# Kernel tuning notes

Hardware: AMD Instinct MI355X
Metric: run time of the kernel (lower is better)

Reference implementation:

```python
import jax, jax.numpy as jnp
import numpy as np

B = 512      # batch
T = 16       # tokens per instruction
V = 1000     # vocab
E = 4        # num_experts
K = 1        # active experts per layer
NLAYERS = 3
TOPK_LOGIC = 32


def _conv(x, w, b, stride=2):
    # x: [B,Cin,H,W], w: [Cout,Cin,3,3] (OIHW), padding=1, stride=2
    y = jax.lax.conv_general_dilated(
        x, w, window_strides=(stride, stride), padding=((1, 1), (1, 1)),
        dimension_numbers=('NCHW', 'OIHW', 'NCHW'))
    return y + b[None, :, None, None]


def _gated_conv(x, w, b, gate):
    # w: [E,Cout,Cin,3,3], b: [E,Cout], gate: [B,E] 0/1 mask
    # Faithful to original: all experts computed densely, then masked.
    outs = jax.vmap(lambda wi, bi: _conv(x, wi, bi))(w, b)  # [E,B,Cout,H',W']
    return jnp.einsum('ebchw,be->bchw', outs, gate)


def _topk_mask(logits, k):
    # 0/1 mask with ones at the top-k positions along the last axis
    _, idx = jax.lax.top_k(logits, k)
    return jnp.sum(jax.nn.one_hot(idx, logits.shape[-1], dtype=logits.dtype), axis=-2)


def setup_inputs() -> dict:
    key = jax.random.key(0)
    ks = jax.random.split(key, 16)
    def rn(k, shape, s=0.05):
        return jax.random.normal(k, shape, jnp.float32) * s
    return dict(
        img=jax.random.normal(ks[0], (B, 12, 56, 56), jnp.float32),
        text=jax.random.randint(ks[1], (B, T), 0, V),
        prev_action=jax.random.randint(ks[2], (B,), 0, 7),
        emb_table=rn(ks[3], (V, 32), 1.0),
        r_w1=rn(ks[4], (32, 64)), r_b1=jnp.zeros((64,), jnp.float32),
        r_w2=rn(ks[5], (64, NLAYERS * E)), r_b2=jnp.zeros((NLAYERS * E,), jnp.float32),
        l_w1=rn(ks[6], (32, 64)), l_b1=jnp.zeros((64,), jnp.float32),
        l_w2=rn(ks[7], (64, 256)), l_b2=jnp.zeros((256,), jnp.float32),
        c1_w=rn(ks[8], (E, 32, 12, 3, 3)), c1_b=jnp.zeros((E, 32), jnp.float32),
        c2_w=rn(ks[9], (E, 64, 32, 3, 3)), c2_b=jnp.zeros((E, 64), jnp.float32),
        c3_w=rn(ks[10], (E, 128, 64, 3, 3)), c3_b=jnp.zeros((E, 128), jnp.float32),
        act_emb=rn(ks[11], (7, 16), 1.0),
        f_w=rn(ks[12], (6272 + 32 + 16, 256)), f_b=jnp.zeros((256,), jnp.float32),
        h_w=rn(ks[13], (256, 5)), h_b=jnp.zeros((5,), jnp.float32),
    )


def reference(img, text, prev_action, emb_table, r_w1, r_b1, r_w2, r_b2,
              l_w1, l_b1, l_w2, l_b2, c1_w, c1_b, c2_w, c2_b, c3_w, c3_b,
              act_emb, f_w, f_b, h_w, h_b):
    # EmbeddingBag(mode='mean') over token dim
    lang = jnp.mean(emb_table[text], axis=1)                      # [B,32]
    # Router: MLP -> [B,3,E] logits, top-k scatter -> 0/1 mask
    rlog = (jax.nn.relu(lang @ r_w1 + r_b1) @ r_w2 + r_b2).reshape(-1, NLAYERS, E)
    masks = _topk_mask(rlog, K)                                   # [B,3,E]
    x = jax.nn.relu(_gated_conv(img, c1_w, c1_b, masks[:, 0, :])) # [B,32,28,28]
    x = jax.nn.relu(_gated_conv(x, c2_w, c2_b, masks[:, 1, :]))   # [B,64,14,14]
    x = jax.nn.relu(_gated_conv(x, c3_w, c3_b, masks[:, 2, :]))   # [B,128,7,7]
    vis = x.reshape(x.shape[0], -1)                               # [B,6272]
    act = act_emb[prev_action]                                    # [B,16]
    fused = jnp.concatenate([vis, lang, act], axis=1)             # [B,6320]
    hidden = fused @ f_w + f_b                                    # [B,256]
    logic = jax.nn.relu(lang @ l_w1 + l_b1) @ l_w2 + l_b2         # [B,256]
    lmask = _topk_mask(logic, TOPK_LOGIC)                         # [B,256]
    out = jax.nn.relu(hidden * lmask)                             # dropout is identity in eval
    logits = out @ h_w + h_b                                      # [B,5]
    return logits, rlog
```

## Files before the change

kernel.cpp:

```cpp
#include <hip/hip_runtime.h>
#include <hip/hip_bf16.h>


typedef __bf16 bf16x8 __attribute__((ext_vector_type(8)));
typedef float f32x4 __attribute__((ext_vector_type(4)));

__device__ __forceinline__ unsigned short f2bf(float f) {
  union { float f; unsigned u; } v; v.f = f;
  unsigned r = v.u + 0x7FFFu + ((v.u >> 16) & 1u);
  return (unsigned short)(r >> 16);
}

__device__ __forceinline__ int wswz(int b) { return b ^ (((b >> 7) & 3) << 4); }

__global__ __launch_bounds__(256) void prep_kernel(
    const int* __restrict__ text, const float* __restrict__ emb,
    const float* __restrict__ r_w1, const float* __restrict__ r_b1,
    const float* __restrict__ r_w2, const float* __restrict__ r_b2,
    const float* __restrict__ l_w1, const float* __restrict__ l_b1,
    const float* __restrict__ l_w2, const float* __restrict__ l_b2,
    const float* __restrict__ act_emb, const int* __restrict__ pa,
    const float* __restrict__ c1_w, const float* __restrict__ c2_w,
    const float* __restrict__ c3_w, const float* __restrict__ fw,
    float* __restrict__ rlog_out, int* __restrict__ eidx, float* __restrict__ lmask,
    unsigned short* __restrict__ tailb,
    unsigned short* __restrict__ wb1, unsigned short* __restrict__ wb2,
    unsigned short* __restrict__ wb3, unsigned short* __restrict__ fwT) {
  __shared__ __align__(16) char shm[64 * 72 * 2];
  const int blk = blockIdx.x;
  const int tid = threadIdx.x;

  if (blk < 512) {
    int b = blk;
    int t = tid;
    __shared__ float lg[32];
    __shared__ float hr[64];
    __shared__ float hl[64];
    __shared__ float rl[12];
    __shared__ float lgc[256];

    if (t < 32) {
      const int* tb = text + b * 16;
      float s = 0.f;
#pragma unroll
      for (int tok = 0; tok < 16; ++tok) s += emb[tb[tok] * 32 + t];
      lg[t] = s * 0.0625f;
    }
    __syncthreads();

    if (t < 64) {
      float s1 = r_b1[t], s2 = l_b1[t];
      for (int k = 0; k < 32; ++k) {
        float lv = lg[k];
        s1 += lv * r_w1[k * 64 + t];
        s2 += lv * l_w1[k * 64 + t];
      }
      hr[t] = fmaxf(s1, 0.f);
      hl[t] = fmaxf(s2, 0.f);
    }
    if (t < 64) {
      float v = 0.f;
      if (t < 32) v = lg[t];
      else if (t < 48) v = act_emb[pa[b] * 16 + (t - 32)];
      tailb[b * 64 + t] = f2bf(v);
    }
    __syncthreads();

    if (t < 12) {
      float s = r_b2[t];
      for (int k = 0; k < 64; ++k) s += hr[k] * r_w2[k * 12 + t];
      rl[t] = s;
      rlog_out[b * 12 + t] = s;
    }
    {
      float s = l_b2[t];
      for (int k = 0; k < 64; ++k) s += hl[k] * l_w2[k * 256 + t];
      lgc[t] = s;
    }
    __syncthreads();

    if (t < 3) {
      int best = 0;
      float bv = rl[t * 4];
      for (int e = 1; e < 4; ++e) {
        float v = rl[t * 4 + e];
        if (v > bv) { bv = v; best = e; }
      }
      eidx[b * 3 + t] = best;
    }
    {
      float v = lgc[t];
      int cnt = 0;
      for (int k = 0; k < 256; ++k) {
        float u = lgc[k];
        cnt += (u > v) || (u == v && k < t);
      }
      lmask[b * 256 + t] = (cnt < 32) ? 1.f : 0.f;
    }
  } else if (blk < 2080) {
    int idx = (blk - 512) * 256 + tid;
    if (idx < 24576) {
      int k = idx % 192, ec = idx / 192;
      float v = 0.f;
      if (k < 144) {
        int g = k >> 4, ci = k & 15;
        if (ci < 12) v = c1_w[ec * 108 + ci * 9 + g];
      }
      wb1[idx] = f2bf(v);
    } else if (idx < 106496) {
      int i2 = idx - 24576;
      int k = i2 % 320, ec = i2 / 320;
      float v = 0.f;
      if (k < 288) {
        int g = k >> 5, ci = k & 31;
        v = c2_w[ec * 288 + ci * 9 + g];
      }
      wb2[i2] = f2bf(v);
    } else {
      int i3 = idx - 106496;
      int k = i3 % 576, ec = i3 / 576;
      int g = k >> 6, ci = k & 63;
      wb3[i3] = f2bf(c3_w[ec * 576 + ci * 9 + g]);
    }
  } else {
    unsigned short(*tl)[72] = (unsigned short(*)[72])shm;
    int fb = blk - 2080;
    int kblk = fb >> 2, nblk = fb & 3;
    int n0 = nblk * 64;
    int k0 = kblk * 64;
    int rl = tid >> 2;
    int c4 = (tid & 3) * 16;
    int srow;
    bool valid;
    if (kblk < 98) {
      int p = kblk >> 1;
      int c0 = (kblk & 1) * 64;
      srow = (c0 + rl) * 49 + p;
      valid = true;
    } else {
      srow = 6272 + rl;
      valid = (rl < 48);
    }
#pragma unroll
    for (int h = 0; h < 4; ++h) {
      float4 v = valid ? *(const float4*)&fw[(size_t)srow * 256 + n0 + c4 + h * 4]
                       : (float4){0.f, 0.f, 0.f, 0.f};
      tl[rl][c4 + h * 4 + 0] = f2bf(v.x);
      tl[rl][c4 + h * 4 + 1] = f2bf(v.y);
      tl[rl][c4 + h * 4 + 2] = f2bf(v.z);
      tl[rl][c4 + h * 4 + 3] = f2bf(v.w);
    }
    __syncthreads();
    int nloc = tid >> 2;
    int kc = (tid & 3) * 16;
    unsigned short vv[16];
#pragma unroll
    for (int i = 0; i < 16; ++i) vv[i] = tl[kc + i][nloc];
    unsigned short* dst = fwT + (size_t)(n0 + nloc) * 6336 + k0 + kc;
    *(uint4*)dst = *(const uint4*)&vv[0];
    *(uint4*)(dst + 8) = *(const uint4*)&vv[8];
  }
}

__global__ __launch_bounds__(256) void bucket_kernel(const int* __restrict__ eidx,
                                                     int* __restrict__ cnt,
                                                     int* __restrict__ perm) {
  int l = blockIdx.x;
  __shared__ int el[512];
  __shared__ int cc[4];
  int t = threadIdx.x;
  el[t] = eidx[t * 3 + l];
  el[t + 256] = eidx[(t + 256) * 3 + l];
  __syncthreads();
  if (t < 4) {
    int c = 0;
    for (int b = 0; b < 512; ++b) c += (el[b] == t);
    cc[t] = c;
    cnt[l * 4 + t] = c;
  }
  __syncthreads();
#pragma unroll
  for (int rep = 0; rep < 2; ++rep) {
    int b = t + rep * 256;
    int e = el[b];
    int rank = 0;
    for (int bp = 0; bp < b; ++bp) rank += (el[bp] == e);
    int off = 0;
    for (int ee = 0; ee < e; ++ee) off += cc[ee];
    perm[l * 512 + off + rank] = b;
  }
}

__global__ __launch_bounds__(256) void conv1_fused(
    const float* __restrict__ img, const unsigned short* __restrict__ wb,
    const float* __restrict__ bias, const int* __restrict__ eidx,
    unsigned short* __restrict__ out) {
  const int s = blockIdx.x / 7;
  const int t = blockIdx.x % 7;
  const int e = eidx[s * 3];
  __shared__ __align__(16) char win[25536];
  __shared__ __align__(16) char ldsB[3 * 4096];
  const int tid = threadIdx.x;
  const int lane = tid & 63;
  const int wid = tid >> 6;
  const int wm0 = wid * 32;

  const int p0 = t * 128;
  const int ohmin = p0 / 28;
  const int ih0 = ohmin * 2 - 1;

  {
    uint4 z; z.x = z.y = z.z = z.w = 0u;
    for (int i = tid; i < 1596; i += 256) ((uint4*)win)[i] = z;
  }
  {
    const unsigned short* wbe = wb + e * (32 * 192);
#pragma unroll
    for (int c = 0; c < 3; ++c) {
      int cc = tid + 256 * c;
      int n = cc / 24, cb = cc - n * 24;
      int kt = cb >> 3, cbl = cb & 7;
      uint4 v = *(const uint4*)(wbe + n * 192 + cb * 8);
      *(uint4*)(ldsB + kt * 4096 + n * 128 + ((cbl * 16) ^ ((n & 7) << 4))) = v;
    }
  }
  __syncthreads();

  for (int task = tid; task < 312; task += 256) {
    int row = task >> 1, half = task & 1;
    int ci = row / 13, ihl = row - ci * 13;
    int ih = ih0 + ihl;
    if ((unsigned)ih < 56u) {
      const float* src = img + (size_t)s * 37632 + ci * 3136 + ih * 56 + half * 28;
      int base = (ihl * 57 + half * 28 + 1) * 32 + ci * 2;
#pragma unroll
      for (int u = 0; u < 7; ++u) {
        float4 v = *(const float4*)(src + u * 4);
        unsigned short w4[4] = {f2bf(v.x), f2bf(v.y), f2bf(v.z), f2bf(v.w)};
#pragma unroll
        for (int q = 0; q < 4; ++q) {
          int bp = base + (u * 4 + q) * 32;
          *(unsigned short*)(win + wswz(bp)) = w4[q];
        }
      }
    }
  }

  int ohl[2], owr[2];
#pragma unroll
  for (int mf = 0; mf < 2; ++mf) {
    int m = wm0 + mf * 16 + (lane & 15);
    int p = p0 + m;
    if (p > 783) p = 783;
    int oh = p / 28;
    owr[mf] = p - oh * 28;
    ohl[mf] = (oh - ohmin) * 2;
  }
  const int lg = lane >> 4;
  const int ci0 = (lg & 1) * 8;
  const int lgh = lg >> 1;
  int brdo[2], brx[2];
#pragma unroll
  for (int nf = 0; nf < 2; ++nf) {
    int n = nf * 16 + (lane & 15);
    brdo[nf] = n * 128;
    brx[nf] = (n & 7) << 4;
  }

  f32x4 acc[2][2];
#pragma unroll
  for (int mf = 0; mf < 2; ++mf)
#pragma unroll
    for (int nf = 0; nf < 2; ++nf) acc[mf][nf] = (f32x4){0.f, 0.f, 0.f, 0.f};

  __syncthreads();

#pragma unroll
  for (int kt = 0; kt < 3; ++kt) {
#pragma unroll
    for (int ks = 0; ks < 2; ++ks) {
      const int g = kt * 4 + ks * 2 + lgh;
      const int kh = g / 3;
      const int kw = g - kh * 3;
      const bool gv = (g < 9);
      bf16x8 af[2];
#pragma unroll
      for (int mf = 0; mf < 2; ++mf) {
        int iwp = owr[mf] * 2 + kw;
        int ihl = ohl[mf] + kh;
        int bp = gv ? ((ihl * 57 + iwp) * 32 + ci0 * 2)
                    : (13 * 57 * 32 + ci0 * 2);
        af[mf] = __builtin_bit_cast(bf16x8, *(const uint4*)(win + wswz(bp)));
      }
      bf16x8 bfv[2];
      const int cb = ks * 64 + ((lane >> 4) << 4);
#pragma unroll
      for (int nf = 0; nf < 2; ++nf)
        bfv[nf] = __builtin_bit_cast(bf16x8,
            *(const uint4*)(ldsB + kt * 4096 + brdo[nf] + (cb ^ brx[nf])));
#pragma unroll
      for (int mf = 0; mf < 2; ++mf)
#pragma unroll
        for (int nf = 0; nf < 2; ++nf)
          acc[mf][nf] = __builtin_amdgcn_mfma_f32_16x16x32_bf16(af[mf], bfv[nf], acc[mf][nf], 0, 0, 0);
    }
  }

  const int col = lane & 15;
  const int rg = (lane >> 4) * 4;
  const float b0 = bias[e * 32 + col];
  const float b1 = bias[e * 32 + 16 + col];
#pragma unroll
  for (int mf = 0; mf < 2; ++mf)
#pragma unroll
    for (int r = 0; r < 4; ++r) {
      int m = wm0 + mf * 16 + rg + r;
      int p = p0 + m;
      if (p < 784) {
        size_t ob = ((size_t)s * 784 + p) * 32;
        out[ob + col]      = f2bf(fmaxf(acc[mf][0][r] + b0, 0.f));
        out[ob + 16 + col] = f2bf(fmaxf(acc[mf][1][r] + b1, 0.f));
      }
    }
}

template<int CIN, int H, int OH, int KREAL, int KP, int COUT,
         int WGM, int WGN, int MF, int NF>
__global__ __launch_bounds__(256) void conv_mfma(
    const unsigned short* __restrict__ in, const unsigned short* __restrict__ wb,
    const float* __restrict__ bias, const int* __restrict__ cnt,
    const int* __restrict__ perm, unsigned short* __restrict__ out) {
  constexpr int PerS = OH * OH;
  constexpr int BM = WGM * MF * 16;
  constexpr int BN = WGN * NF * 16;
  constexpr int AJ = BM / 32;
  constexpr int KT = KP / 64;
  constexpr int W = H;
  constexpr int BCH = BN / 32;

  int bm = blockIdx.x;
  int e = 0, row0 = 0, rows = 0;
  bool found = false;
  {
    int acc = 0, ebase = 0;
#pragma unroll
    for (int ee = 0; ee < 4; ++ee) {
      int er = cnt[ee] * PerS;
      int te = (er + BM - 1) / BM;
      if (!found && bm < acc + te) {
        e = ee;
        row0 = ebase + (bm - acc) * BM;
        rows = er - (bm - acc) * BM;
        if (rows > BM) rows = BM;
        found = true;
      }
      acc += te;
      ebase += er;
    }
  }
  if (!found) return;

  __shared__ __align__(16) char lds[BM * 128 + BN * 128];
  char* ldsB = lds + BM * 128;
  const int tid = threadIdx.x;
  const int lane = tid & 63;
  const int wid = tid >> 6;
  const int wm0 = (wid / WGN) * (MF * 16);
  const int wn0 = (wid % WGN) * (NF * 16);
  const int c16 = tid & 7;

  int ihc[AJ], iwc[AJ], abase[AJ], adso[AJ];
#pragma unroll
  for (int j = 0; j < AJ; ++j) {
    int r = (tid >> 3) + 32 * j;
    int gr = row0 + r;
    const int MAXR = 512 * PerS - 1;
    if (gr > MAXR) gr = MAXR;
    int sord = gr / PerS;
    int p = gr - sord * PerS;
    int s = perm[sord];
    int oh = p / OH, ow = p - oh * OH;
    ihc[j] = oh * 2 - 1;
    iwc[j] = ow * 2 - 1;
    abase[j] = s * (H * W);
    adso[j] = r * 128 + ((c16 * 16) ^ ((r & 7) << 4));
  }
  const unsigned short* wbe = wb + (size_t)e * COUT * KP;
  int bgo[BCH], bdso[BCH];
#pragma unroll
  for (int c = 0; c < BCH; ++c) {
    int cc = tid + 256 * c;
    int n = cc >> 3, cb = cc & 7;
    bgo[c] = n * KP + cb * 8;
    bdso[c] = n * 128 + ((cb * 16) ^ ((n & 7) << 4));
  }
  int ardo[MF], arx[MF], brdo[NF], brx[NF];
#pragma unroll
  for (int mf = 0; mf < MF; ++mf) {
    int r = wm0 + mf * 16 + (lane & 15);
    ardo[mf] = r * 128;
    arx[mf] = (r & 7) << 4;
  }
#pragma unroll
  for (int nf = 0; nf < NF; ++nf) {
    int n = wn0 + nf * 16 + (lane & 15);
    brdo[nf] = n * 128;
    brx[nf] = (n & 7) << 4;
  }

  auto loadA = [&](int kt, int j) -> uint4 {
    uint4 z; z.x = z.y = z.z = z.w = 0u;
    int kbase = kt * 64 + c16 * 8;
    if (kbase >= KREAL) return z;
    int g = kbase / CIN;
    int ci0 = kbase - g * CIN;
    int kh = g / 3, kw = g - (g / 3) * 3;
    int ih = ihc[j] + kh, iw = iwc[j] + kw;
    if ((unsigned)ih >= (unsigned)H || (unsigned)iw >= (unsigned)W) return z;
    const unsigned short* p = in + ((size_t)(abase[j] + ih * W + iw) * CIN + ci0);
    return *(const uint4*)p;
  };

  uint4 rA[AJ], rB[BCH];
#pragma unroll
  for (int j = 0; j < AJ; ++j) rA[j] = loadA(0, j);
#pragma unroll
  for (int c = 0; c < BCH; ++c) rB[c] = *(const uint4*)(wbe + bgo[c]);

  f32x4 acc[MF][NF];
#pragma unroll
  for (int mf = 0; mf < MF; ++mf)
#pragma unroll
    for (int nf = 0; nf < NF; ++nf) acc[mf][nf] = (f32x4){0.f, 0.f, 0.f, 0.f};

  for (int kt = 0; kt < KT; ++kt) {
    __syncthreads();
#pragma unroll
    for (int j = 0; j < AJ; ++j) *(uint4*)(lds + adso[j]) = rA[j];
#pragma unroll
    for (int c = 0; c < BCH; ++c) *(uint4*)(ldsB + bdso[c]) = rB[c];
    __syncthreads();
    if (kt + 1 < KT) {
#pragma unroll
      for (int j = 0; j < AJ; ++j) rA[j] = loadA(kt + 1, j);
#pragma unroll
      for (int c = 0; c < BCH; ++c) rB[c] = *(const uint4*)(wbe + bgo[c] + (kt + 1) * 64);
    }
#pragma unroll
    for (int ks = 0; ks < 2; ++ks) {
      int cb = ks * 64 + ((lane >> 4) << 4);
      bf16x8 af[MF], bfv[NF];
#pragma unroll
      for (int mf = 0; mf < MF; ++mf)
        af[mf] = __builtin_bit_cast(bf16x8, *(const uint4*)(lds + ardo[mf] + (cb ^ arx[mf])));
#pragma unroll
      for (int nf = 0; nf < NF; ++nf)
        bfv[nf] = __builtin_bit_cast(bf16x8, *(const uint4*)(ldsB + brdo[nf] + (cb ^ brx[nf])));
#pragma unroll
      for (int mf = 0; mf < MF; ++mf)
#pragma unroll
        for (int nf = 0; nf < NF; ++nf)
          acc[mf][nf] = __builtin_amdgcn_mfma_f32_16x16x32_bf16(af[mf], bfv[nf], acc[mf][nf], 0, 0, 0);
    }
  }

  const int col = lane & 15;
  const int rg = (lane >> 4) * 4;
#pragma unroll
  for (int mf = 0; mf < MF; ++mf) {
#pragma unroll
    for (int r = 0; r < 4; ++r) {
      int m = wm0 + mf * 16 + rg + r;
      if (m < rows) {
        int gr = row0 + m;
        int sord = gr / PerS;
        int p = gr - sord * PerS;
        int s = perm[sord];
        size_t ob = ((size_t)s * PerS + p) * COUT;
#pragma unroll
        for (int nf = 0; nf < NF; ++nf) {
          int co = wn0 + nf * 16 + col;
          float v = acc[mf][nf][r] + bias[e * COUT + co];
          out[ob + co] = f2bf(fmaxf(v, 0.f));
        }
      }
    }
  }
}

__global__ __launch_bounds__(256) void fgemm_kernel(
    const unsigned short* __restrict__ x3, const unsigned short* __restrict__ tail,
    const unsigned short* __restrict__ fwT, float* __restrict__ partial) {
  constexpr int MF = 2, NF = 2;
  const int row0 = blockIdx.x * 64;
  const int nc0 = blockIdx.y * 64;
  const int kz = blockIdx.z * 704;
  __shared__ __align__(16) char lds[64 * 128 + 64 * 128];
  char* ldsB = lds + 64 * 128;
  const int tid = threadIdx.x;
  const int lane = tid & 63;
  const int wid = tid >> 6;
  const int wm0 = (wid >> 1) * 32;
  const int wn0 = (wid & 1) * 32;
  const int c16 = tid & 7;
  int arow[2], adso[2];
#pragma unroll
  for (int j = 0; j < 2; ++j) {
    int r = (tid >> 3) + 32 * j;
    arow[j] = row0 + r;
    adso[j] = r * 128 + ((c16 * 16) ^ ((r & 7) << 4));
  }
  int bgo[2], bdso[2];
#pragma unroll
  for (int c = 0; c < 2; ++c) {
    int cc = tid + 256 * c;
    int n = cc >> 3, cb = cc & 7;
    bgo[c] = (nc0 + n) * 6336 + kz + cb * 8;
    bdso[c] = n * 128 + ((cb * 16) ^ ((n & 7) << 4));
  }
  int ardo[MF], arx[MF], brdo[NF], brx[NF];
#pragma unroll
  for (int mf = 0; mf < MF; ++mf) {
    int r = wm0 + mf * 16 + (lane & 15);
    ardo[mf] = r * 128; arx[mf] = (r & 7) << 4;
  }
#pragma unroll
  for (int nf = 0; nf < NF; ++nf) {
    int n = wn0 + nf * 16 + (lane & 15);
    brdo[nf] = n * 128; brx[nf] = (n & 7) << 4;
  }
  auto loadA = [&](int kt, int j) -> uint4 {
    int k = kz + kt * 64 + c16 * 8;
    const unsigned short* p;
    if (k < 6272) p = x3 + (size_t)arow[j] * 6272 + k;
    else p = tail + arow[j] * 64 + (k - 6272);
    return *(const uint4*)p;
  };
  uint4 rA[2], rB[2];
#pragma unroll
  for (int j = 0; j < 2; ++j) rA[j] = loadA(0, j);
#pragma unroll
  for (int c = 0; c < 2; ++c) rB[c] = *(const uint4*)(fwT + bgo[c]);
  f32x4 acc[MF][NF];
#pragma unroll
  for (int mf = 0; mf < MF; ++mf)
#pragma unroll
    for (int nf = 0; nf < NF; ++nf) acc[mf][nf] = (f32x4){0.f, 0.f, 0.f, 0.f};

  for (int kt = 0; kt < 11; ++kt) {
    __syncthreads();
#pragma unroll
    for (int j = 0; j < 2; ++j) *(uint4*)(lds + adso[j]) = rA[j];
#pragma unroll
    for (int c = 0; c < 2; ++c) *(uint4*)(ldsB + bdso[c]) = rB[c];
    __syncthreads();
    if (kt + 1 < 11) {
#pragma unroll
      for (int j = 0; j < 2; ++j) rA[j] = loadA(kt + 1, j);
#pragma unroll
      for (int c = 0; c < 2; ++c) rB[c] = *(const uint4*)(fwT + bgo[c] + (kt + 1) * 64);
    }
#pragma unroll
    for (int ks = 0; ks < 2; ++ks) {
      int cb = ks * 64 + ((lane >> 4) << 4);
      bf16x8 af[MF], bfv[NF];
#pragma unroll
      for (int mf = 0; mf < MF; ++mf)
        af[mf] = __builtin_bit_cast(bf16x8, *(const uint4*)(lds + ardo[mf] + (cb ^ arx[mf])));
#pragma unroll
      for (int nf = 0; nf < NF; ++nf)
        bfv[nf] = __builtin_bit_cast(bf16x8, *(const uint4*)(ldsB + brdo[nf] + (cb ^ brx[nf])));
#pragma unroll
      for (int mf = 0; mf < MF; ++mf)
#pragma unroll
        for (int nf = 0; nf < NF; ++nf)
          acc[mf][nf] = __builtin_amdgcn_mfma_f32_16x16x32_bf16(af[mf], bfv[nf], acc[mf][nf], 0, 0, 0);
    }
  }
  const int col = lane & 15;
  const int rg = (lane >> 4) * 4;
  float* pz = partial + (size_t)blockIdx.z * 131072;
#pragma unroll
  for (int mf = 0; mf < MF; ++mf)
#pragma unroll
    for (int r = 0; r < 4; ++r) {
      int m = wm0 + mf * 16 + rg + r;
      int grow = row0 + m;
#pragma unroll
      for (int nf = 0; nf < NF; ++nf) {
        int n = nc0 + wn0 + nf * 16 + col;
        pz[grow * 256 + n] = acc[mf][nf][r];
      }
    }
}

__global__ __launch_bounds__(256) void reduce_head(const float* __restrict__ part,
                                                   const float* __restrict__ f_b,
                                                   const float* __restrict__ lmask,
                                                   const float* __restrict__ h_w,
                                                   const float* __restrict__ h_b,
                                                   float* __restrict__ logits) {
  int b = blockIdx.x, t = threadIdx.x;
  float s = f_b[t];
#pragma unroll
  for (int z = 0; z < 9; ++z) s += part[z * 131072 + b * 256 + t];
  __shared__ float o[256];
  o[t] = (lmask[b * 256 + t] != 0.f) ? fmaxf(s, 0.f) : 0.f;
  __syncthreads();
  if (t < 5) {
    float v = h_b[t];
    for (int n = 0; n < 256; ++n) v += o[n] * h_w[n * 5 + t];
    logits[b * 5 + t] = v;
  }
}

extern "C" void kernel_launch(void* const* d_in, const int* in_sizes, int n_in,
                              void* d_out, int out_size, void* d_ws, size_t ws_size,
                              hipStream_t stream) {
  (void)in_sizes; (void)n_in; (void)out_size; (void)ws_size;
  const float* img       = (const float*)d_in[0];
  const int*   text      = (const int*)d_in[1];
  const int*   pa        = (const int*)d_in[2];
  const float* emb_table = (const float*)d_in[3];
  const float* r_w1 = (const float*)d_in[4];
  const float* r_b1 = (const float*)d_in[5];
  const float* r_w2 = (const float*)d_in[6];
  const float* r_b2 = (const float*)d_in[7];
  const float* l_w1 = (const float*)d_in[8];
  const float* l_b1 = (const float*)d_in[9];
  const float* l_w2 = (const float*)d_in[10];
  const float* l_b2 = (const float*)d_in[11];
  const float* c1_w = (const float*)d_in[12];
  const float* c1_b = (const float*)d_in[13];
  const float* c2_w = (const float*)d_in[14];
  const float* c2_b = (const float*)d_in[15];
  const float* c3_w = (const float*)d_in[16];
  const float* c3_b = (const float*)d_in[17];
  const float* act_emb = (const float*)d_in[18];
  const float* f_w = (const float*)d_in[19];
  const float* f_b = (const float*)d_in[20];
  const float* h_w = (const float*)d_in[21];
  const float* h_b = (const float*)d_in[22];

  float* outf   = (float*)d_out;
  float* logits = outf;
  float* rlog   = outf + 2560;

  char* cur = (char*)d_ws;
  auto alloc = [&](size_t bytes) { char* r = cur; cur += (bytes + 255) & ~(size_t)255; return r; };
  float* lmask   = (float*)alloc(131072 * 4);
  int* eidx      = (int*)alloc(1536 * 4);
  int* cnt       = (int*)alloc(12 * 4);
  int* perm      = (int*)alloc(1536 * 4);
  unsigned short* wb1  = (unsigned short*)alloc((size_t)24576 * 2);
  unsigned short* wb2  = (unsigned short*)alloc((size_t)81920 * 2);
  unsigned short* wb3  = (unsigned short*)alloc((size_t)294912 * 2);
  unsigned short* fwT  = (unsigned short*)alloc((size_t)1622016 * 2);
  unsigned short* tailb= (unsigned short*)alloc((size_t)32768 * 2);
  unsigned short* x1b  = (unsigned short*)alloc((size_t)12845056 * 2);
  unsigned short* x2b  = (unsigned short*)alloc((size_t)6422528 * 2);
  unsigned short* x3b  = (unsigned short*)alloc((size_t)3211264 * 2);
  float* partial       = (float*)alloc((size_t)9 * 131072 * 4);

  prep_kernel<<<2476, 256, 0, stream>>>(text, emb_table,
                                        r_w1, r_b1, r_w2, r_b2,
                                        l_w1, l_b1, l_w2, l_b2,
                                        act_emb, pa,
                                        c1_w, c2_w, c3_w, f_w,
                                        rlog, eidx, lmask, tailb,
                                        wb1, wb2, wb3, fwT);
  bucket_kernel<<<3, 256, 0, stream>>>(eidx, cnt, perm);

  conv1_fused<<<3584, 256, 0, stream>>>(img, wb1, c1_b, eidx, x1b);
  conv_mfma<32, 28, 14, 288, 320, 64, 2, 2, 4, 2>
      <<<787, 256, 0, stream>>>(x1b, wb2, c2_b, cnt + 4, perm + 512, x2b);
  conv_mfma<64, 14, 7, 576, 576, 128, 1, 4, 4, 2>
      <<<395, 256, 0, stream>>>(x2b, wb3, c3_b, cnt + 8, perm + 1024, x3b);

  fgemm_kernel<<<dim3(8, 4, 9), 256, 0, stream>>>(x3b, tailb, fwT, partial);
  reduce_head<<<512, 256, 0, stream>>>(partial, f_b, lmask, h_w, h_b, logits);
}
```

Baseline: 148.0 us.

## Retile conv1 to half-sample blocks with larger LDS window and more fragments per wave

Conv1 now runs one block per half image (392 output pixels) instead of seven 128-pixel tiles per sample. Each block stages a 29-row input window, reused across 25 M-fragments, with each wave handling up to 7 fragments. This amortizes weight staging and halo rows over more output and cuts the block count. The image load is also rewritten to gather four channels per thread into 8-byte LDS stores. In exchange, LDS per block rises to about 68 KB and the accumulator arrays grow, which lowers occupancy, and one wave is partly idle because 25 fragments do not split evenly across 4 waves.

Result: slower. 172.8 us (+16.8%).

```diff
diff --git a/kernel.cpp b/kernel.cpp
--- a/kernel.cpp
+++ b/kernel.cpp
@@ -191,27 +191,25 @@
   }
 }
 
-__global__ __launch_bounds__(256) void conv1_fused(
+__global__ __launch_bounds__(256) void conv1_sample(
     const float* __restrict__ img, const unsigned short* __restrict__ wb,
     const float* __restrict__ bias, const int* __restrict__ eidx,
     unsigned short* __restrict__ out) {
-  const int s = blockIdx.x / 7;
-  const int t = blockIdx.x % 7;
+  const int s = blockIdx.x >> 1;
+  const int h = blockIdx.x & 1;
   const int e = eidx[s * 3];
-  __shared__ __align__(16) char win[25536];
+  __shared__ __align__(16) char win[55680];
   __shared__ __align__(16) char ldsB[3 * 4096];
   const int tid = threadIdx.x;
   const int lane = tid & 63;
   const int wid = tid >> 6;
-  const int wm0 = wid * 32;
-
-  const int p0 = t * 128;
-  const int ohmin = p0 / 28;
-  const int ih0 = ohmin * 2 - 1;
+
+  const int p0 = h * 392;
+  const int ih0 = h * 28 - 1;
 
   {
     uint4 z; z.x = z.y = z.z = z.w = 0u;
-    for (int i = tid; i < 1596; i += 256) ((uint4*)win)[i] = z;
+    for (int i = tid; i < 3480; i += 256) ((uint4*)win)[i] = z;
   }
   {
     const unsigned short* wbe = wb + e * (32 * 192);
@@ -226,50 +224,47 @@
   }
   __syncthreads();
 
-  for (int task = tid; task < 312; task += 256) {
-    int row = task >> 1, half = task & 1;
-    int ci = row / 13, ihl = row - ci * 13;
+  const float* ibase = img + (size_t)s * 37632;
+  for (int c = tid; c < 4872; c += 256) {
+    int q = c / 1624;
+    int rem = c - q * 1624;
+    int ihl = rem / 56;
+    int iw = rem - ihl * 56;
     int ih = ih0 + ihl;
     if ((unsigned)ih < 56u) {
-      const float* src = img + (size_t)s * 37632 + ci * 3136 + ih * 56 + half * 28;
-      int base = (ihl * 57 + half * 28 + 1) * 32 + ci * 2;
-#pragma unroll
-      for (int u = 0; u < 7; ++u) {
-        float4 v = *(const float4*)(src + u * 4);
-        unsigned short w4[4] = {f2bf(v.x), f2bf(v.y), f2bf(v.z), f2bf(v.w)};
-#pragma unroll
-        for (int q = 0; q < 4; ++q) {
-          int bp = base + (u * 4 + q) * 32;
-          *(unsigned short*)(win + wswz(bp)) = w4[q];
-        }
-      }
-    }
-  }
-
-  int ohl[2], owr[2];
-#pragma unroll
-  for (int mf = 0; mf < 2; ++mf) {
-    int m = wm0 + mf * 16 + (lane & 15);
-    int p = p0 + m;
-    if (p > 783) p = 783;
-    int oh = p / 28;
-    owr[mf] = p - oh * 28;
-    ohl[mf] = (oh - ohmin) * 2;
-  }
+      const float* src = ibase + q * 4 * 3136 + ih * 56 + iw;
+      unsigned short w4[4] = {f2bf(src[0]), f2bf(src[3136]),
+                              f2bf(src[6272]), f2bf(src[9408])};
+      int bp = (ihl * 58 + iw + 1) * 32 + q * 8;
+      *(unsigned long long*)(win + wswz(bp)) = *(const unsigned long long*)w4;
+    }
+  }
+
+  const int colr = lane & 15;
   const int lg = lane >> 4;
   const int ci0 = (lg & 1) * 8;
   const int lgh = lg >> 1;
+  int ohl2[7], owr2[7];
+#pragma unroll
+  for (int mf = 0; mf < 7; ++mf) {
+    int frag = wid * 7 + mf;
+    int m = frag * 16 + colr;
+    if (m > 391) m = 391;
+    int ohl = m / 28;
+    owr2[mf] = (m - ohl * 28) * 2;
+    ohl2[mf] = ohl * 2;
+  }
   int brdo[2], brx[2];
 #pragma unroll
   for (int nf = 0; nf < 2; ++nf) {
-    int n = nf * 16 + (lane & 15);
+    int n = nf * 16 + colr;
     brdo[nf] = n * 128;
     brx[nf] = (n & 7) << 4;
   }
 
-  f32x4 acc[2][2];
-#pragma unroll
-  for (int mf = 0; mf < 2; ++mf)
+  f32x4 acc[7][2];
+#pragma unroll
+  for (int mf = 0; mf < 7; ++mf)
 #pragma unroll
     for (int nf = 0; nf < 2; ++nf) acc[mf][nf] = (f32x4){0.f, 0.f, 0.f, 0.f};
 
@@ -283,45 +278,50 @@
       const int kh = g / 3;
       const int kw = g - kh * 3;
       const bool gv = (g < 9);
-      bf16x8 af[2];
-#pragma unroll
-      for (int mf = 0; mf < 2; ++mf) {
-        int iwp = owr[mf] * 2 + kw;
-        int ihl = ohl[mf] + kh;
-        int bp = gv ? ((ihl * 57 + iwp) * 32 + ci0 * 2)
-                    : (13 * 57 * 32 + ci0 * 2);
-        af[mf] = __builtin_bit_cast(bf16x8, *(const uint4*)(win + wswz(bp)));
-      }
       bf16x8 bfv[2];
-      const int cb = ks * 64 + ((lane >> 4) << 4);
+      const int cb = ks * 64 + (lg << 4);
 #pragma unroll
       for (int nf = 0; nf < 2; ++nf)
         bfv[nf] = __builtin_bit_cast(bf16x8,
             *(const uint4*)(ldsB + kt * 4096 + brdo[nf] + (cb ^ brx[nf])));
-#pragma unroll
-      for (int mf = 0; mf < 2; ++mf)
-#pragma unroll
-        for (int nf = 0; nf < 2; ++nf)
-          acc[mf][nf] = __builtin_amdgcn_mfma_f32_16x16x32_bf16(af[mf], bfv[nf], acc[mf][nf], 0, 0, 0);
-    }
-  }
-
-  const int col = lane & 15;
-  const int rg = (lane >> 4) * 4;
-  const float b0 = bias[e * 32 + col];
-  const float b1 = bias[e * 32 + 16 + col];
-#pragma unroll
-  for (int mf = 0; mf < 2; ++mf)
-#pragma unroll
-    for (int r = 0; r < 4; ++r) {
-      int m = wm0 + mf * 16 + rg + r;
-      int p = p0 + m;
-      if (p < 784) {
-        size_t ob = ((size_t)s * 784 + p) * 32;
-        out[ob + col]      = f2bf(fmaxf(acc[mf][0][r] + b0, 0.f));
-        out[ob + 16 + col] = f2bf(fmaxf(acc[mf][1][r] + b1, 0.f));
-      }
-    }
+      bf16x8 af[7];
+#pragma unroll
+      for (int mf = 0; mf < 7; ++mf) {
+        if (wid * 7 + mf < 25) {
+          int bp = gv ? (((ohl2[mf] + kh) * 58 + owr2[mf] + kw) * 32 + ci0 * 2)
+                      : (29 * 58 * 32 + ci0 * 2);
+          af[mf] = __builtin_bit_cast(bf16x8, *(const uint4*)(win + wswz(bp)));
+        }
+      }
+#pragma unroll
+      for (int mf = 0; mf < 7; ++mf) {
+        if (wid * 7 + mf < 25) {
+#pragma unroll
+          for (int nf = 0; nf < 2; ++nf)
+            acc[mf][nf] = __builtin_amdgcn_mfma_f32_16x16x32_bf16(af[mf], bfv[nf], acc[mf][nf], 0, 0, 0);
+        }
+      }
+    }
+  }
+
+  const float b0 = bias[e * 32 + colr];
+  const float b1 = bias[e * 32 + 16 + colr];
+  const int rg = lg * 4;
+#pragma unroll
+  for (int mf = 0; mf < 7; ++mf) {
+    int frag = wid * 7 + mf;
+    if (frag < 25) {
+#pragma unroll
+      for (int r = 0; r < 4; ++r) {
+        int m = frag * 16 + rg + r;
+        if (m < 392) {
+          size_t ob = ((size_t)s * 784 + p0 + m) * 32;
+          out[ob + colr]      = f2bf(fmaxf(acc[mf][0][r] + b0, 0.f));
+          out[ob + 16 + colr] = f2bf(fmaxf(acc[mf][1][r] + b1, 0.f));
+        }
+      }
+    }
+  }
 }
 
 template<int CIN, int H, int OH, int KREAL, int KP, int COUT,
@@ -671,7 +671,7 @@
                                         wb1, wb2, wb3, fwT);
   bucket_kernel<<<3, 256, 0, stream>>>(eidx, cnt, perm);
 
-  conv1_fused<<<3584, 256, 0, stream>>>(img, wb1, c1_b, eidx, x1b);
+  conv1_sample<<<1024, 256, 0, stream>>>(img, wb1, c1_b, eidx, x1b);
   conv_mfma<32, 28, 14, 288, 320, 64, 2, 2, 4, 2>
       <<<787, 256, 0, stream>>>(x1b, wb2, c2_b, cnt + 4, perm + 512, x2b);
   conv_mfma<64, 14, 7, 576, 576, 128, 1, 4, 4, 2>
```
